# Optimization experiments

Hardware: AMD Instinct MI355X
Metric: run time of the kernel (lower is better)

The kernel has to match this reference:

```python
import jax, jax.numpy as jnp
import numpy as np

C = 64
OUT_Z = 32
HW = 128
NUM_HEADS = 4
COMP = 16          # max(c//reduction, num_heads) = 64//4
HEAD_DIM = COMP // NUM_HEADS
MAX_Z = 32
GROWTH = 16
NEG_SLOPE = 0.2


def setup_inputs() -> dict:
    key = jax.random.key(0)
    ks = jax.random.split(key, 16)
    ch = OUT_Z * C  # 2048

    def nrm(k, shape, std):
        return (jax.random.normal(k, shape, jnp.float32) * std).astype(jnp.float32)

    inp = {
        "trans_feature": jax.random.normal(ks[0], (1, ch, HW, HW), jnp.float32),
        "ln_w": jnp.ones((C,), jnp.float32),
        "ln_b": jnp.zeros((C,), jnp.float32),
        "wq": nrm(ks[1], (C, COMP), 0.05), "bq": jnp.zeros((COMP,), jnp.float32),
        "wk": nrm(ks[2], (C, COMP), 0.05), "bk": jnp.zeros((COMP,), jnp.float32),
        "wv": nrm(ks[3], (C, COMP), 0.05), "bv": jnp.zeros((COMP,), jnp.float32),
        "wo": nrm(ks[4], (COMP, C), 0.05), "bo": jnp.zeros((C,), jnp.float32),
        "rel_z_bias": nrm(ks[5], (NUM_HEADS, 2 * MAX_Z + 1), 0.02),
        "attn_gamma": jnp.asarray(0.1, jnp.float32),
        "dw0": nrm(ks[6], (ch + 0 * GROWTH, GROWTH), 0.02), "db0": jnp.zeros((GROWTH,), jnp.float32),
        "dw1": nrm(ks[7], (ch + 1 * GROWTH, GROWTH), 0.02), "db1": jnp.zeros((GROWTH,), jnp.float32),
        "dw2": nrm(ks[8], (ch + 2 * GROWTH, GROWTH), 0.02), "db2": jnp.zeros((GROWTH,), jnp.float32),
        "fuse_w": nrm(ks[9], (ch + 3 * GROWTH, ch), 0.02), "fuse_b": jnp.zeros((ch,), jnp.float32),
        "rdc_scale": jnp.asarray(0.1, jnp.float32),
        "out_z": OUT_Z,
    }
    return inp


def _conv1x1(x, w, b):
    # 1x1 conv == per-pixel dense: x [B,Cin,H,W], w [Cin,Cout]
    return jnp.einsum('bchw,co->bohw', x, w) + b[None, :, None, None]


def _lrelu(x):
    return jnp.where(x >= 0, x, NEG_SLOPE * x)


def reference(trans_feature, ln_w, ln_b, wq, bq, wk, bk, wv, bv, wo, bo,
              rel_z_bias, attn_gamma, dw0, db0, dw1, db1, dw2, db2,
              fuse_w, fuse_b, rdc_scale, out_z):
    B, Ct, H, W = trans_feature.shape
    c = Ct // out_z
    # ---- ZAxisAttention on slices [out_z, c, H, W] ----
    x = trans_feature.reshape(out_z, c, H, W)
    xf = x.transpose(0, 2, 3, 1).reshape(out_z, H * W, c)   # [Z, N, c]
    mu = xf.mean(-1, keepdims=True)
    var = ((xf - mu) ** 2).mean(-1, keepdims=True)
    normed = (xf - mu) * jax.lax.rsqrt(var + 1e-5) * ln_w + ln_b
    pooled = normed.mean(1)                                  # [Z, c]
    q = (pooled @ wq + bq).reshape(out_z, NUM_HEADS, HEAD_DIM).transpose(1, 0, 2)
    k = (pooled @ wk + bk).reshape(out_z, NUM_HEADS, HEAD_DIM).transpose(1, 0, 2)
    v = (pooled @ wv + bv).reshape(out_z, NUM_HEADS, HEAD_DIM).transpose(1, 0, 2)
    attn = jnp.einsum('hid,hjd->hij', q, k) * (HEAD_DIM ** -0.5)  # [h, Z, Z]
    zr = jnp.arange(out_z)
    rel_idx = jnp.clip(zr[None, :] - zr[:, None] + MAX_Z, 0, 2 * MAX_Z)
    attn = jax.nn.softmax(attn + rel_z_bias[:, rel_idx], axis=-1)
    o = jnp.einsum('hij,hjd->hid', attn, v).transpose(1, 0, 2).reshape(out_z, COMP)
    o = o @ wo + bo                                          # [Z, c]
    x_z = (x + attn_gamma * o[:, :, None, None]).reshape(B, Ct, H, W)
    # ---- ResidualDenseBlock on full [B, Ct, H, W] (out_z == max_out_z) ----
    feats = trans_feature
    f0 = _lrelu(_conv1x1(feats, dw0, db0))
    feats = jnp.concatenate([feats, f0], axis=1)
    f1 = _lrelu(_conv1x1(feats, dw1, db1))
    feats = jnp.concatenate([feats, f1], axis=1)
    f2 = _lrelu(_conv1x1(feats, dw2, db2))
    feats = jnp.concatenate([feats, f2], axis=1)
    fused = _lrelu(_conv1x1(feats, fuse_w, fuse_b))
    x_rdc = trans_feature + rdc_scale * fused
    return x_z + x_rdc - trans_feature
```

## Files before the change

### kernel.cpp

```cpp
#include <hip/hip_runtime.h>
#include <hip/hip_fp8.h>

typedef unsigned char u8;
typedef unsigned short u16;
typedef long lng2 __attribute__((ext_vector_type(2)));
typedef float f32x4 __attribute__((ext_vector_type(4)));
typedef u16 u16x8 __attribute__((ext_vector_type(8)));
typedef u8 u8x16 __attribute__((ext_vector_type(16)));

#define HW_N 16384
#define NCH  2048

__device__ __forceinline__ u16 f2bf(float f) {
  union { float f; unsigned u; } v; v.f = f;
  unsigned r = v.u + 0x7FFFu + ((v.u >> 16) & 1u);
  return (u16)(r >> 16);
}
__device__ __forceinline__ float bf2f(u16 u) {
  union { unsigned u; float f; } v; v.u = ((unsigned)u) << 16; return v.f;
}
__device__ __forceinline__ u8 f2fp8(float f) {
  __hip_fp8_e4m3 t(f);
  return (u8)t.__x;
}
__device__ __forceinline__ float lrelu(float v) { return v >= 0.0f ? v : 0.2f * v; }

__device__ __forceinline__ void gload_lds16(const u8* g, u8* l) {
  __builtin_amdgcn_global_load_lds((const __attribute__((address_space(1))) void*)g,
                                   (__attribute__((address_space(3))) void*)l, 16, 0, 0);
}

__global__ __launch_bounds__(256) void k_stats(const float* __restrict__ trans,
                                               u8* __restrict__ A8,
                                               float* __restrict__ pooled_sum) {
  const int z = blockIdx.x;
  const int tid = threadIdx.x;
  const int ptile = blockIdx.y;
  const int p = ptile * 256 + tid;
  const float* src = trans + (size_t)z * 64 * HW_N + p;
  float x[64];
#pragma unroll
  for (int c = 0; c < 64; ++c) x[c] = src[(size_t)c * HW_N];
  float sum = 0.f, sq = 0.f;
#pragma unroll
  for (int c = 0; c < 64; ++c) { sum += x[c]; sq += x[c] * x[c]; }
  const float mu = sum * (1.0f / 64.0f);
  const float var = sq * (1.0f / 64.0f) - mu * mu;
  const float rstd = rsqrtf(var + 1e-5f);

  __shared__ __align__(16) u8 rawt[256 * 64];
  __shared__ __align__(16) u16 normt[256 * 64];
  const int r3m = tid & 3, r7 = tid & 7;
#pragma unroll
  for (int c = 0; c < 4; ++c) {
    u8x16 y;
#pragma unroll
    for (int w = 0; w < 16; ++w) {
      const int k = (w < 8) ? (c * 8 + w) : (32 + c * 8 + (w - 8));
      y[w] = f2fp8(x[k]);
    }
    *(u8x16*)&rawt[tid * 64 + ((c ^ r3m) << 4)] = y;
  }
#pragma unroll
  for (int c8 = 0; c8 < 8; ++c8) {
    u16x8 wn;
#pragma unroll
    for (int e = 0; e < 8; ++e) wn[e] = f2bf((x[c8 * 8 + e] - mu) * rstd);
    *(u16x8*)&normt[tid * 64 + ((c8 ^ r7) << 3)] = wn;
  }
  __syncthreads();

  u8* gbase = A8 + ((size_t)z * HW_N + (size_t)ptile * 256) * 64;
#pragma unroll
  for (int it = 0; it < 4; ++it) {
    const int o = it * 256 + tid;
    const int row = o >> 2, c4 = o & 3;
    *(u8x16*)(gbase + o * 16) = *(const u8x16*)&rawt[row * 64 + ((c4 ^ (row & 3)) << 4)];
  }

  const int c = tid & 63, q = tid >> 6;
  const int kc2 = c >> 3, e2 = c & 7;
  float s = 0.f;
#pragma unroll 8
  for (int i = 0; i < 64; ++i) {
    const int row = q * 64 + i;
    s += bf2f(normt[row * 64 + ((kc2 ^ (row & 7)) << 3) + e2]);
  }
  __shared__ float red2[4][64];
  red2[q][c] = s;
  __syncthreads();
  if (tid < 64) {
    atomicAdd(&pooled_sum[z * 64 + tid],
              red2[0][tid] + red2[1][tid] + red2[2][tid] + red2[3][tid]);
  }
}

__global__ __launch_bounds__(256) void k_wpack(const float* __restrict__ fw,
                                               const float* __restrict__ dw0,
                                               const float* __restrict__ dw1,
                                               const float* __restrict__ dw2,
                                               u8* __restrict__ W8,
                                               u8* __restrict__ Wd8) {
  __shared__ float tile[64][65];
  const int tid = threadIdx.x;
  const int ktile = blockIdx.x;
  const int yb = blockIdx.y;
  if (yb == 32) {
    const int kc = ktile;
    if (kc >= 32) return;
    for (int idx = tid; idx < 3072; idx += 256) {
      const int kk = idx / 48, j = idx % 48;
      const int k = kc * 64 + kk;
      float v = (j < 16) ? dw0[k * 16 + j]
              : (j < 32) ? dw1[k * 16 + (j - 16)]
                         : dw2[k * 16 + (j - 32)];
      tile[kk][j] = v;
    }
    __syncthreads();
    for (int idx = tid; idx < 3072; idx += 256) {
      const int j = idx / 64, kk = idx % 64;
      const int pos = ((kk >> 3) & 3) * 16 + (kk & 7) + ((kk >> 5) << 3);
      Wd8[((size_t)kc * 48 + j) * 64 + pos] = f2fp8(16.0f * tile[kk][j]);
    }
    return;
  }
  const int ntile = yb;
  {
    const int kk0 = tid >> 6, nn = tid & 63;
#pragma unroll
    for (int it = 0; it < 16; ++it) {
      int kk = it * 4 + kk0;
      int kg = ktile * 64 + kk;
      tile[kk][nn] = (kg < 2096) ? fw[(size_t)kg * NCH + ntile * 64 + nn] : 0.0f;
    }
  }
  __syncthreads();
  {
    const int kk = tid & 63, nn0 = tid >> 6;
    const int pos = ((kk >> 3) & 3) * 16 + (kk & 7) + ((kk >> 5) << 3);
#pragma unroll
    for (int it = 0; it < 16; ++it) {
      int n = it * 4 + nn0;
      W8[((size_t)ktile * NCH + ntile * 64 + n) * 64 + pos] = f2fp8(16.0f * tile[kk][n]);
    }
  }
}

__global__ __launch_bounds__(256) void k_dense(const u8* __restrict__ A8,
    const u8* __restrict__ Wd8,
    const float* __restrict__ dw1, const float* __restrict__ dw2,
    const float* __restrict__ db0, const float* __restrict__ db1,
    const float* __restrict__ db2, u8* __restrict__ A8out) {
  __shared__ __align__(16) u8 lsA[128 * 64];
  __shared__ __align__(16) u8 lsW[48 * 64];
  __shared__ float trn[128][49];
  __shared__ float w1t[16][16];
  __shared__ float w2t[32][16];
  __shared__ float biases[48];
  const int tid = threadIdx.x;
  const int lane = tid & 63;
  const int wave = __builtin_amdgcn_readfirstlane(tid >> 6);
  const int mb = blockIdx.x;
  const int r16 = lane & 15, kgrp = lane >> 4;
  const int sgoff8 = ((lane >> 2) << 6) + (((lane & 3) ^ ((lane >> 3) & 3)) << 4);
  const int kx = (kgrp ^ ((r16 >> 1) & 3)) << 4;

  if (tid < 256) w1t[tid >> 4][tid & 15] = dw1[(2048 + (tid >> 4)) * 16 + (tid & 15)];
  for (int idx = tid; idx < 512; idx += 256)
    w2t[idx >> 4][idx & 15] = dw2[(2048 + (idx >> 4)) * 16 + (idx & 15)];
  if (tid < 48) biases[tid] = (tid < 16) ? db0[tid] : (tid < 32) ? db1[tid - 16] : db2[tid - 32];

  f32x4 acc[3][2] = {};
  for (int t = 0; t < 32; ++t) {
    const u8* slabA = A8 + ((size_t)t * HW_N + (size_t)mb * 128) * 64;
    const u8* slabW = Wd8 + (size_t)t * 48 * 64;
#pragma unroll
    for (int p = 0; p < 2; ++p)
      gload_lds16(slabA + (p * 4 + wave) * 1024 + sgoff8, lsA + (p * 4 + wave) * 1024);
    if (wave < 3)
      gload_lds16(slabW + wave * 1024 + sgoff8, lsW + wave * 1024);
    asm volatile("s_waitcnt vmcnt(0)" ::: "memory");
    __syncthreads();

    lng2 wf[3], af[2];
#pragma unroll
    for (int f = 0; f < 3; ++f)
      wf[f] = *(const lng2*)(lsW + (f * 16 + r16) * 64 + kx);
#pragma unroll
    for (int g = 0; g < 2; ++g)
      af[g] = *(const lng2*)(lsA + (wave * 32 + g * 16 + r16) * 64 + kx);
#pragma unroll
    for (int f = 0; f < 3; ++f)
#pragma unroll
      for (int g = 0; g < 2; ++g) {
        acc[f][g] = __builtin_amdgcn_mfma_f32_16x16x32_fp8_fp8(wf[f][0], af[g][0], acc[f][g], 0, 0, 0);
        acc[f][g] = __builtin_amdgcn_mfma_f32_16x16x32_fp8_fp8(wf[f][1], af[g][1], acc[f][g], 0, 0, 0);
      }
    __syncthreads();
  }

  const int rg = lane >> 4;
#pragma unroll
  for (int f = 0; f < 3; ++f)
#pragma unroll
    for (int r = 0; r < 4; ++r)
#pragma unroll
      for (int g = 0; g < 2; ++g)
        trn[wave * 32 + g * 16 + r16][f * 16 + rg * 4 + r] = acc[f][g][r] * 0.0625f;
  __syncthreads();

  if (tid < 128) {
    float gv[48];
#pragma unroll
    for (int j = 0; j < 48; ++j) gv[j] = trn[tid][j];
    float f0[16], f1[16], f2[16];
#pragma unroll
    for (int j = 0; j < 16; ++j) f0[j] = lrelu(gv[j] + biases[j]);
#pragma unroll
    for (int j = 0; j < 16; ++j) {
      float a = gv[16 + j] + biases[16 + j];
#pragma unroll
      for (int i = 0; i < 16; ++i) a += f0[i] * w1t[i][j];
      f1[j] = lrelu(a);
    }
#pragma unroll
    for (int j = 0; j < 16; ++j) {
      float a = gv[32 + j] + biases[32 + j];
#pragma unroll
      for (int i = 0; i < 16; ++i) a += f0[i] * w2t[i][j];
#pragma unroll
      for (int i = 0; i < 16; ++i) a += f1[i] * w2t[16 + i][j];
      f2[j] = lrelu(a);
    }
    u8* dst = A8out + ((size_t)32 * HW_N + mb * 128 + tid) * 64;
#pragma unroll
    for (int c = 0; c < 4; ++c) {
      u8x16 y;
#pragma unroll
      for (int w = 0; w < 16; ++w) {
        const int k = (w < 8) ? (c * 8 + w) : (32 + c * 8 + (w - 8));
        const float v = (k < 16) ? f0[k] : (k < 32) ? f1[k - 16] : (k < 48) ? f2[k - 32] : 0.0f;
        y[w] = f2fp8(v);
      }
      *(u8x16*)(dst + c * 16) = y;
    }
  }
}

__global__ __launch_bounds__(256) void k_attn(const float* __restrict__ pooled_sum,
    const float* __restrict__ ln_w, const float* __restrict__ ln_b,
    const float* __restrict__ wq, const float* __restrict__ bq,
    const float* __restrict__ wk, const float* __restrict__ bk,
    const float* __restrict__ wv, const float* __restrict__ bv,
    const float* __restrict__ wo, const float* __restrict__ bo,
    const float* __restrict__ relz, const float* __restrict__ attn_gamma,
    float* __restrict__ o_scaled) {
  __shared__ float pooled[2048];
  __shared__ float q[512], k[512], v[512], att[4096], tz[512];
  const int tid = threadIdx.x;
  for (int i = tid; i < 2048; i += 256) {
    int c = i & 63;
    pooled[i] = ln_w[c] * pooled_sum[i] * (1.0f / 16384.0f) + ln_b[c];
  }
  __syncthreads();
  for (int i = tid; i < 512; i += 256) {
    int z = i >> 4, e = i & 15;
    float aq = bq[e], ak = bk[e], av = bv[e];
    for (int c = 0; c < 64; ++c) {
      float p = pooled[z * 64 + c];
      aq += p * wq[c * 16 + e]; ak += p * wk[c * 16 + e]; av += p * wv[c * 16 + e];
    }
    q[i] = aq; k[i] = ak; v[i] = av;
  }
  __syncthreads();
  if (tid < 128) {
    int h = tid >> 5, zi = tid & 31;
    float s[32]; float mx = -1e30f;
#pragma unroll
    for (int j = 0; j < 32; ++j) {
      float d = 0.f;
#pragma unroll
      for (int e = 0; e < 4; ++e) d += q[zi * 16 + h * 4 + e] * k[j * 16 + h * 4 + e];
      d = d * 0.5f + relz[h * 65 + (j - zi + 32)];
      s[j] = d; mx = fmaxf(mx, d);
    }
    float ssum = 0.f;
#pragma unroll
    for (int j = 0; j < 32; ++j) { s[j] = __expf(s[j] - mx); ssum += s[j]; }
    float inv = 1.0f / ssum;
#pragma unroll
    for (int j = 0; j < 32; ++j) att[(h * 32 + zi) * 32 + j] = s[j] * inv;
  }
  __syncthreads();
  for (int i = tid; i < 512; i += 256) {
    int z = i >> 4, hd = i & 15, h = hd >> 2;
    float a = 0.f;
    for (int j = 0; j < 32; ++j) a += att[(h * 32 + z) * 32 + j] * v[j * 16 + hd];
    tz[i] = a;
  }
  __syncthreads();
  const float gamma = attn_gamma[0];
  for (int i = tid; i < 2048; i += 256) {
    int z = i >> 6, c = i & 63;
    float a = bo[c];
    for (int hd = 0; hd < 16; ++hd) a += tz[z * 16 + hd] * wo[hd * 64 + c];
    o_scaled[i] = gamma * a;
  }
}

__global__ __launch_bounds__(512, 2) void k_gemm(
    const u8* __restrict__ A8, const u8* __restrict__ W8,
    const float* __restrict__ trans, const float* __restrict__ o_scaled,
    const float* __restrict__ fuse_b, const float* __restrict__ rdc_scale,
    float* __restrict__ out) {
  __shared__ __align__(16) u8 ls[65536];
  const int tid = threadIdx.x;
  const int lane = tid & 63;
  const int wave = __builtin_amdgcn_readfirstlane(tid >> 6);
  const int bid = blockIdx.x;
  const int nb = bid & 7;
  const int mb = bid >> 3;
  const int mbase = mb * 256, nbase = nb * 256;
  const int wm = wave & 1;
  const int wn = wave >> 1;
  const int wnh = wn >> 1;
  const int wrow = (wn & 1) * 64;
  const int r16 = lane & 15, kgrp = lane >> 4;
  const int sgoff8 = ((lane >> 2) << 6) + (((lane & 3) ^ ((lane >> 3) & 3)) << 4);
  const int kx = (kgrp ^ ((r16 >> 1) & 3)) << 4;

#define LA(b, h) (ls + (b) * 32768 + (h) * 8192)
#define LW(b, h) (ls + (b) * 32768 + 16384 + (h) * 8192)
#define AHALF(t, h) (A8 + ((size_t)(t) * HW_N + mbase + (h) * 128) * 64)
#define WHALF(t, h) (W8 + ((size_t)(t) * NCH + nbase + (h) * 128) * 64)
#define STAGE(rows, ldsh) gload_lds16((rows) + wave * 1024 + sgoff8, (ldsh) + wave * 1024)
#define RD8(base, row) (*(const lng2*)((base) + (row) * 64 + kx))
#define MF8(a, b, c) __builtin_amdgcn_mfma_f32_16x16x32_fp8_fp8((a), (b), (c), 0, 0, 0)

  f32x4 acc[4][8] = {};
  lng2 wf0a[2], afLa[4];
  lng2 wf0b[2], afLb[4];

  STAGE(WHALF(0, 0), LW(0, 0));
  STAGE(WHALF(0, 1), LW(0, 1));
  STAGE(AHALF(0, 0), LA(0, 0));
  STAGE(AHALF(0, 1), LA(0, 1));
  asm volatile("s_waitcnt vmcnt(0)" ::: "memory");
  __builtin_amdgcn_s_barrier();
  {
    const u8* lw0 = LW(0, wnh);
    const u8* la0 = LA(0, wm);
#pragma unroll
    for (int f = 0; f < 2; ++f) wf0a[f] = RD8(lw0, wrow + f * 16 + r16);
#pragma unroll
    for (int g = 0; g < 4; ++g) afLa[g] = RD8(la0, g * 16 + r16);
  }

#define GBODY(T, W0C, ALC, W0N, ALN)                                           \
  {                                                                            \
    const int t = (T);                                                         \
    const int buf = t & 1, nbf = buf ^ 1;                                      \
    const int tn = (t + 1 < 33) ? t + 1 : 32;                                  \
    const u8* la = LA(buf, wm);                                                \
    const u8* lw = LW(buf, wnh);                                               \
    lng2 wf1[2], afH[4];                                                       \
                            \
    _Pragma("unroll") for (int f = 0; f < 2; ++f)                              \
      wf1[f] = RD8(lw, wrow + 32 + f * 16 + r16);                              \
    STAGE(WHALF(tn, 0), LW(nbf, 0));                                           \
    STAGE(WHALF(tn, 1), LW(nbf, 1));                                           \
    __builtin_amdgcn_s_setprio(1);                                             \
    _Pragma("unroll") for (int f = 0; f < 2; ++f)                              \
      _Pragma("unroll") for (int g = 0; g < 4; ++g) {                          \
        acc[f][g] = MF8(W0C[f][0], ALC[g][0], acc[f][g]);                      \
        acc[f][g] = MF8(W0C[f][1], ALC[g][1], acc[f][g]);                      \
      }                                                                        \
    __builtin_amdgcn_s_setprio(0);                                             \
                            \
    _Pragma("unroll") for (int g = 0; g < 4; ++g)                              \
      afH[g] = RD8(la, 64 + g * 16 + r16);                                     \
    STAGE(AHALF(tn, 0), LA(nbf, 0));                                           \
    STAGE(AHALF(tn, 1), LA(nbf, 1));                                           \
    __builtin_amdgcn_s_setprio(1);                                             \
    _Pragma("unroll") for (int f = 0; f < 2; ++f)                              \
      _Pragma("unroll") for (int g = 0; g < 4; ++g) {                          \
        acc[2 + f][g] = MF8(wf1[f][0], ALC[g][0], acc[2 + f][g]);              \
        acc[2 + f][g] = MF8(wf1[f][1], ALC[g][1], acc[2 + f][g]);              \
      }                                                                        \
    __builtin_amdgcn_s_setprio(0);                                             \
                                            \
    __builtin_amdgcn_s_setprio(1);                                             \
    _Pragma("unroll") for (int f = 0; f < 2; ++f)                              \
      _Pragma("unroll") for (int g = 0; g < 4; ++g) {                          \
        acc[2 + f][4 + g] = MF8(wf1[f][0], afH[g][0], acc[2 + f][4 + g]);      \
        acc[2 + f][4 + g] = MF8(wf1[f][1], afH[g][1], acc[2 + f][4 + g]);      \
      }                                                                        \
    __builtin_amdgcn_s_setprio(0);                                             \
            \
    asm volatile("s_waitcnt vmcnt(0)" ::: "memory");                           \
    __builtin_amdgcn_s_barrier();                                              \
    {                                                                          \
      const u8* lan = LA(nbf, wm);                                             \
      const u8* lwn = LW(nbf, wnh);                                            \
      _Pragma("unroll") for (int f = 0; f < 2; ++f)                            \
        W0N[f] = RD8(lwn, wrow + f * 16 + r16);                                \
      _Pragma("unroll") for (int g = 0; g < 4; ++g)                            \
        ALN[g] = RD8(lan, g * 16 + r16);                                       \
    }                                                                          \
    __builtin_amdgcn_s_setprio(1);                                             \
    _Pragma("unroll") for (int f = 0; f < 2; ++f)                              \
      _Pragma("unroll") for (int g = 0; g < 4; ++g) {                          \
        acc[f][4 + g] = MF8(W0C[f][0], afH[g][0], acc[f][4 + g]);              \
        acc[f][4 + g] = MF8(W0C[f][1], afH[g][1], acc[f][4 + g]);              \
      }                                                                        \
    __builtin_amdgcn_s_setprio(0);                                             \
  }

  for (int u = 0; u < 16; ++u) {
    GBODY(2 * u, wf0a, afLa, wf0b, afLb);
    GBODY(2 * u + 1, wf0b, afLb, wf0a, afLa);
  }
  GBODY(32, wf0a, afLa, wf0b, afLb);

  asm volatile("s_waitcnt vmcnt(0)" ::: "memory");

  const float rdc = rdc_scale[0];
  const int rg = lane >> 4;
#pragma unroll
  for (int f = 0; f < 4; ++f) {
#pragma unroll
    for (int r = 0; r < 4; ++r) {
      const int row = nbase + wn * 64 + f * 16 + rg * 4 + r;
      const float ob = o_scaled[row], fb = fuse_b[row];
#pragma unroll
      for (int g = 0; g < 8; ++g) {
        const int col = mbase + wm * 128 + g * 16 + r16;
        float v = lrelu(acc[f][g][r] * 0.0625f + fb);
        const size_t idx = (size_t)row * HW_N + col;
        out[idx] = trans[idx] + rdc * v + ob;
      }
    }
  }
#undef GBODY
#undef LA
#undef LW
#undef AHALF
#undef WHALF
#undef STAGE
#undef RD8
#undef MF8
}

extern "C" void kernel_launch(void* const* d_in, const int* in_sizes, int n_in,
                              void* d_out, int out_size, void* d_ws, size_t ws_size,
                              hipStream_t stream) {
  (void)in_sizes; (void)n_in; (void)out_size; (void)ws_size;
  const float* trans = (const float*)d_in[0];
  const float* ln_w  = (const float*)d_in[1];
  const float* ln_b  = (const float*)d_in[2];
  const float* wq = (const float*)d_in[3];  const float* bq = (const float*)d_in[4];
  const float* wk = (const float*)d_in[5];  const float* bk = (const float*)d_in[6];
  const float* wv = (const float*)d_in[7];  const float* bv = (const float*)d_in[8];
  const float* wo = (const float*)d_in[9];  const float* bo = (const float*)d_in[10];
  const float* relz  = (const float*)d_in[11];
  const float* gamma = (const float*)d_in[12];
  const float* dw0 = (const float*)d_in[13]; const float* db0 = (const float*)d_in[14];
  const float* dw1 = (const float*)d_in[15]; const float* db1 = (const float*)d_in[16];
  const float* dw2 = (const float*)d_in[17]; const float* db2 = (const float*)d_in[18];
  const float* fuse_w = (const float*)d_in[19];
  const float* fuse_b = (const float*)d_in[20];
  const float* rdc    = (const float*)d_in[21];
  float* out = (float*)d_out;

  char* ws = (char*)d_ws;
  u8*    A8         = (u8*)ws;
  u8*    W8         = (u8*)(ws + 34603008);
  u8*    Wd8        = (u8*)(ws + 38928384);
  float* pooled_sum = (float*)(ws + 39026688);
  float* o_scaled   = (float*)(ws + 39034880);

  hipMemsetAsync(pooled_sum, 0, 2048 * sizeof(float), stream);
  k_stats<<<dim3(32, 64), 256, 0, stream>>>(trans, A8, pooled_sum);
  k_wpack<<<dim3(33, 33), 256, 0, stream>>>(fuse_w, dw0, dw1, dw2, W8, Wd8);
  k_dense<<<dim3(128), 256, 0, stream>>>(A8, Wd8, dw1, dw2, db0, db1, db2, A8);
  k_attn<<<dim3(1), 256, 0, stream>>>(pooled_sum, ln_w, ln_b, wq, bq, wk, bk, wv, bv,
                                      wo, bo, relz, gamma, o_scaled);
  k_gemm<<<dim3(512), 512, 0, stream>>>(A8, W8, trans, o_scaled, fuse_b, rdc, out);
}
```

Measured before the change: 206.1 us.

## Switch FP8 GEMMs to 16x16x128 scaled MFMA with 128-byte K slabs

Repacks the activations and weights into 128-wide K slabs with an XOR-swizzled LDS layout. The dense and fused GEMMs now use the gfx950 mfma_scale 16x16x128 f8f6f4 instruction, which cuts the MFMA issue count and the number of K iterations. The hand-pipelined, double-buffered k_gemm loop is replaced by a simple single-buffered load/wait/compute loop, so global loads no longer overlap with MFMA work. Two extra memsets zero the padding slabs.

```diff
diff --git a/kernel.cpp b/kernel.cpp
--- a/kernel.cpp
+++ b/kernel.cpp
@@ -3,7 +3,8 @@
 
 typedef unsigned char u8;
 typedef unsigned short u16;
-typedef long lng2 __attribute__((ext_vector_type(2)));
+typedef int i32x4 __attribute__((ext_vector_type(4)));
+typedef int i32x8 __attribute__((ext_vector_type(8)));
 typedef float f32x4 __attribute__((ext_vector_type(4)));
 typedef u16 u16x8 __attribute__((ext_vector_type(8)));
 typedef u8 u8x16 __attribute__((ext_vector_type(16)));
@@ -30,8 +31,19 @@
                                    (__attribute__((address_space(3))) void*)l, 16, 0, 0);
 }
 
+#define MFS(a, b, c) \
+  __builtin_amdgcn_mfma_scale_f32_16x16x128_f8f6f4((a), (b), (c), 0, 0, 0, 0x7F7F7F7F, 0, 0x7F7F7F7F)
+
+#define RDFRAG(R, row, kg_, outv)                                              \
+  {                                                                            \
+    const int off_ = ((row) << 7) + ((((kg_) << 1) ^ ((row) & 7)) << 4);       \
+    i32x4 lo_ = *(const i32x4*)((R) + off_);                                   \
+    i32x4 hi_ = *(const i32x4*)((R) + (off_ ^ 16));                            \
+    outv = __builtin_shufflevector(lo_, hi_, 0, 1, 2, 3, 4, 5, 6, 7);          \
+  }
+
 __global__ __launch_bounds__(256) void k_stats(const float* __restrict__ trans,
-                                               u8* __restrict__ A8,
+                                               u8* __restrict__ A16,
                                                float* __restrict__ pooled_sum) {
   const int z = blockIdx.x;
   const int tid = threadIdx.x;
@@ -55,10 +67,7 @@
   for (int c = 0; c < 4; ++c) {
     u8x16 y;
 #pragma unroll
-    for (int w = 0; w < 16; ++w) {
-      const int k = (w < 8) ? (c * 8 + w) : (32 + c * 8 + (w - 8));
-      y[w] = f2fp8(x[k]);
-    }
+    for (int w = 0; w < 16; ++w) y[w] = f2fp8(x[c * 16 + w]);
     *(u8x16*)&rawt[tid * 64 + ((c ^ r3m) << 4)] = y;
   }
 #pragma unroll
@@ -70,12 +79,13 @@
   }
   __syncthreads();
 
-  u8* gbase = A8 + ((size_t)z * HW_N + (size_t)ptile * 256) * 64;
+  u8* gbase = A16 + ((size_t)(z >> 1) * HW_N + (size_t)ptile * 256) * 128 + (z & 1) * 64;
 #pragma unroll
   for (int it = 0; it < 4; ++it) {
     const int o = it * 256 + tid;
     const int row = o >> 2, c4 = o & 3;
-    *(u8x16*)(gbase + o * 16) = *(const u8x16*)&rawt[row * 64 + ((c4 ^ (row & 3)) << 4)];
+    *(u8x16*)(gbase + (size_t)row * 128 + c4 * 16) =
+        *(const u8x16*)&rawt[row * 64 + ((c4 ^ (row & 3)) << 4)];
   }
 
   const int c = tid & 63, q = tid >> 6;
@@ -99,8 +109,8 @@
                                                const float* __restrict__ dw0,
                                                const float* __restrict__ dw1,
                                                const float* __restrict__ dw2,
-                                               u8* __restrict__ W8,
-                                               u8* __restrict__ Wd8) {
+                                               u8* __restrict__ W16,
+                                               u8* __restrict__ Wd16) {
   __shared__ float tile[64][65];
   const int tid = threadIdx.x;
   const int ktile = blockIdx.x;
@@ -119,8 +129,7 @@
     __syncthreads();
     for (int idx = tid; idx < 3072; idx += 256) {
       const int j = idx / 64, kk = idx % 64;
-      const int pos = ((kk >> 3) & 3) * 16 + (kk & 7) + ((kk >> 5) << 3);
-      Wd8[((size_t)kc * 48 + j) * 64 + pos] = f2fp8(16.0f * tile[kk][j]);
+      Wd16[((size_t)(kc >> 1) * 48 + j) * 128 + (kc & 1) * 64 + kk] = f2fp8(16.0f * tile[kk][j]);
     }
     return;
   }
@@ -137,22 +146,22 @@
   __syncthreads();
   {
     const int kk = tid & 63, nn0 = tid >> 6;
-    const int pos = ((kk >> 3) & 3) * 16 + (kk & 7) + ((kk >> 5) << 3);
 #pragma unroll
     for (int it = 0; it < 16; ++it) {
       int n = it * 4 + nn0;
-      W8[((size_t)ktile * NCH + ntile * 64 + n) * 64 + pos] = f2fp8(16.0f * tile[kk][n]);
-    }
-  }
-}
-
-__global__ __launch_bounds__(256) void k_dense(const u8* __restrict__ A8,
-    const u8* __restrict__ Wd8,
+      W16[((size_t)(ktile >> 1) * NCH + ntile * 64 + n) * 128 + (ktile & 1) * 64 + kk] =
+          f2fp8(16.0f * tile[kk][n]);
+    }
+  }
+}
+
+__global__ __launch_bounds__(256) void k_dense(const u8* __restrict__ A16,
+    const u8* __restrict__ Wd16,
     const float* __restrict__ dw1, const float* __restrict__ dw2,
     const float* __restrict__ db0, const float* __restrict__ db1,
-    const float* __restrict__ db2, u8* __restrict__ A8out) {
-  __shared__ __align__(16) u8 lsA[128 * 64];
-  __shared__ __align__(16) u8 lsW[48 * 64];
+    const float* __restrict__ db2, u8* __restrict__ A16out) {
+  __shared__ __align__(16) u8 lsA[128 * 128];
+  __shared__ __align__(16) u8 lsW[48 * 128];
   __shared__ float trn[128][49];
   __shared__ float w1t[16][16];
   __shared__ float w2t[32][16];
@@ -161,9 +170,9 @@
   const int lane = tid & 63;
   const int wave = __builtin_amdgcn_readfirstlane(tid >> 6);
   const int mb = blockIdx.x;
-  const int r16 = lane & 15, kgrp = lane >> 4;
-  const int sgoff8 = ((lane >> 2) << 6) + (((lane & 3) ^ ((lane >> 3) & 3)) << 4);
-  const int kx = (kgrp ^ ((r16 >> 1) & 3)) << 4;
+  const int r16 = lane & 15, kg = lane >> 4;
+  const int srow8 = lane >> 3;
+  const int schunk = (((lane & 7) ^ srow8) << 4);
 
   if (tid < 256) w1t[tid >> 4][tid & 15] = dw1[(2048 + (tid >> 4)) * 16 + (tid & 15)];
   for (int idx = tid; idx < 512; idx += 256)
@@ -171,31 +180,34 @@
   if (tid < 48) biases[tid] = (tid < 16) ? db0[tid] : (tid < 32) ? db1[tid - 16] : db2[tid - 32];
 
   f32x4 acc[3][2] = {};
-  for (int t = 0; t < 32; ++t) {
-    const u8* slabA = A8 + ((size_t)t * HW_N + (size_t)mb * 128) * 64;
-    const u8* slabW = Wd8 + (size_t)t * 48 * 64;
-#pragma unroll
-    for (int p = 0; p < 2; ++p)
-      gload_lds16(slabA + (p * 4 + wave) * 1024 + sgoff8, lsA + (p * 4 + wave) * 1024);
-    if (wave < 3)
-      gload_lds16(slabW + wave * 1024 + sgoff8, lsW + wave * 1024);
+  for (int t = 0; t < 16; ++t) {
+    const u8* Asl = A16 + ((size_t)t * HW_N + (size_t)mb * 128) * 128;
+    const u8* Wsl = Wd16 + (size_t)t * 48 * 128;
+#pragma unroll
+    for (int i = 0; i < 4; ++i) {
+      const int r0 = wave * 32 + i * 8;
+      gload_lds16(Asl + (size_t)(r0 + srow8) * 128 + schunk, lsA + r0 * 128 + lane * 16);
+    }
+    if (wave < 3) {
+#pragma unroll
+      for (int i = 0; i < 2; ++i) {
+        const int r0 = wave * 16 + i * 8;
+        gload_lds16(Wsl + (size_t)(r0 + srow8) * 128 + schunk, lsW + r0 * 128 + lane * 16);
+      }
+    }
     asm volatile("s_waitcnt vmcnt(0)" ::: "memory");
     __syncthreads();
 
-    lng2 wf[3], af[2];
+    i32x8 wf[3], af[2];
+#pragma unroll
+    for (int f = 0; f < 3; ++f) RDFRAG(lsW, f * 16 + r16, kg, wf[f]);
+#pragma unroll
+    for (int g = 0; g < 2; ++g) RDFRAG(lsA, wave * 32 + g * 16 + r16, kg, af[g]);
 #pragma unroll
     for (int f = 0; f < 3; ++f)
-      wf[f] = *(const lng2*)(lsW + (f * 16 + r16) * 64 + kx);
-#pragma unroll
-    for (int g = 0; g < 2; ++g)
-      af[g] = *(const lng2*)(lsA + (wave * 32 + g * 16 + r16) * 64 + kx);
-#pragma unroll
-    for (int f = 0; f < 3; ++f)
-#pragma unroll
-      for (int g = 0; g < 2; ++g) {
-        acc[f][g] = __builtin_amdgcn_mfma_f32_16x16x32_fp8_fp8(wf[f][0], af[g][0], acc[f][g], 0, 0, 0);
-        acc[f][g] = __builtin_amdgcn_mfma_f32_16x16x32_fp8_fp8(wf[f][1], af[g][1], acc[f][g], 0, 0, 0);
-      }
+#pragma unroll
+      for (int g = 0; g < 2; ++g)
+        acc[f][g] = MFS(wf[f], af[g], acc[f][g]);
     __syncthreads();
   }
 
@@ -232,14 +244,14 @@
       for (int i = 0; i < 16; ++i) a += f1[i] * w2t[16 + i][j];
       f2[j] = lrelu(a);
     }
-    u8* dst = A8out + ((size_t)32 * HW_N + mb * 128 + tid) * 64;
-#pragma unroll
-    for (int c = 0; c < 4; ++c) {
+    u8* dst = A16out + ((size_t)16 * HW_N + mb * 128 + tid) * 128;
+#pragma unroll
+    for (int c = 0; c < 3; ++c) {
       u8x16 y;
 #pragma unroll
       for (int w = 0; w < 16; ++w) {
-        const int k = (w < 8) ? (c * 8 + w) : (32 + c * 8 + (w - 8));
-        const float v = (k < 16) ? f0[k] : (k < 32) ? f1[k - 16] : (k < 48) ? f2[k - 32] : 0.0f;
+        const int k = c * 16 + w;
+        const float v = (k < 16) ? f0[k] : (k < 32) ? f1[k - 16] : f2[k - 32];
         y[w] = f2fp8(v);
       }
       *(u8x16*)(dst + c * 16) = y;
@@ -309,7 +321,7 @@
 }
 
 __global__ __launch_bounds__(512, 2) void k_gemm(
-    const u8* __restrict__ A8, const u8* __restrict__ W8,
+    const u8* __restrict__ A16, const u8* __restrict__ W16,
     const float* __restrict__ trans, const float* __restrict__ o_scaled,
     const float* __restrict__ fuse_b, const float* __restrict__ rdc_scale,
     float* __restrict__ out) {
@@ -323,106 +335,45 @@
   const int mbase = mb * 256, nbase = nb * 256;
   const int wm = wave & 1;
   const int wn = wave >> 1;
-  const int wnh = wn >> 1;
-  const int wrow = (wn & 1) * 64;
-  const int r16 = lane & 15, kgrp = lane >> 4;
-  const int sgoff8 = ((lane >> 2) << 6) + (((lane & 3) ^ ((lane >> 3) & 3)) << 4);
-  const int kx = (kgrp ^ ((r16 >> 1) & 3)) << 4;
-
-#define LA(b, h) (ls + (b) * 32768 + (h) * 8192)
-#define LW(b, h) (ls + (b) * 32768 + 16384 + (h) * 8192)
-#define AHALF(t, h) (A8 + ((size_t)(t) * HW_N + mbase + (h) * 128) * 64)
-#define WHALF(t, h) (W8 + ((size_t)(t) * NCH + nbase + (h) * 128) * 64)
-#define STAGE(rows, ldsh) gload_lds16((rows) + wave * 1024 + sgoff8, (ldsh) + wave * 1024)
-#define RD8(base, row) (*(const lng2*)((base) + (row) * 64 + kx))
-#define MF8(a, b, c) __builtin_amdgcn_mfma_f32_16x16x32_fp8_fp8((a), (b), (c), 0, 0, 0)
+  const int r16 = lane & 15, kg = lane >> 4;
+  const int srow8 = lane >> 3;
+  const int schunk = (((lane & 7) ^ srow8) << 4);
+  u8* const lsA = ls;
+  u8* const lsW = ls + 32768;
 
   f32x4 acc[4][8] = {};
-  lng2 wf0a[2], afLa[4];
-  lng2 wf0b[2], afLb[4];
-
-  STAGE(WHALF(0, 0), LW(0, 0));
-  STAGE(WHALF(0, 1), LW(0, 1));
-  STAGE(AHALF(0, 0), LA(0, 0));
-  STAGE(AHALF(0, 1), LA(0, 1));
-  asm volatile("s_waitcnt vmcnt(0)" ::: "memory");
-  __builtin_amdgcn_s_barrier();
-  {
-    const u8* lw0 = LW(0, wnh);
-    const u8* la0 = LA(0, wm);
-#pragma unroll
-    for (int f = 0; f < 2; ++f) wf0a[f] = RD8(lw0, wrow + f * 16 + r16);
-#pragma unroll
-    for (int g = 0; g < 4; ++g) afLa[g] = RD8(la0, g * 16 + r16);
-  }
-
-#define GBODY(T, W0C, ALC, W0N, ALN)                                           \
-  {                                                                            \
-    const int t = (T);                                                         \
-    const int buf = t & 1, nbf = buf ^ 1;                                      \
-    const int tn = (t + 1 < 33) ? t + 1 : 32;                                  \
-    const u8* la = LA(buf, wm);                                                \
-    const u8* lw = LW(buf, wnh);                                               \
-    lng2 wf1[2], afH[4];                                                       \
-                            \
-    _Pragma("unroll") for (int f = 0; f < 2; ++f)                              \
-      wf1[f] = RD8(lw, wrow + 32 + f * 16 + r16);                              \
-    STAGE(WHALF(tn, 0), LW(nbf, 0));                                           \
-    STAGE(WHALF(tn, 1), LW(nbf, 1));                                           \
-    __builtin_amdgcn_s_setprio(1);                                             \
-    _Pragma("unroll") for (int f = 0; f < 2; ++f)                              \
-      _Pragma("unroll") for (int g = 0; g < 4; ++g) {                          \
-        acc[f][g] = MF8(W0C[f][0], ALC[g][0], acc[f][g]);                      \
-        acc[f][g] = MF8(W0C[f][1], ALC[g][1], acc[f][g]);                      \
-      }                                                                        \
-    __builtin_amdgcn_s_setprio(0);                                             \
-                            \
-    _Pragma("unroll") for (int g = 0; g < 4; ++g)                              \
-      afH[g] = RD8(la, 64 + g * 16 + r16);                                     \
-    STAGE(AHALF(tn, 0), LA(nbf, 0));                                           \
-    STAGE(AHALF(tn, 1), LA(nbf, 1));                                           \
-    __builtin_amdgcn_s_setprio(1);                                             \
-    _Pragma("unroll") for (int f = 0; f < 2; ++f)                              \
-      _Pragma("unroll") for (int g = 0; g < 4; ++g) {                          \
-        acc[2 + f][g] = MF8(wf1[f][0], ALC[g][0], acc[2 + f][g]);              \
-        acc[2 + f][g] = MF8(wf1[f][1], ALC[g][1], acc[2 + f][g]);              \
-      }                                                                        \
-    __builtin_amdgcn_s_setprio(0);                                             \
-                                            \
-    __builtin_amdgcn_s_setprio(1);                                             \
-    _Pragma("unroll") for (int f = 0; f < 2; ++f)                              \
-      _Pragma("unroll") for (int g = 0; g < 4; ++g) {                          \
-        acc[2 + f][4 + g] = MF8(wf1[f][0], afH[g][0], acc[2 + f][4 + g]);      \
-        acc[2 + f][4 + g] = MF8(wf1[f][1], afH[g][1], acc[2 + f][4 + g]);      \
-      }                                                                        \
-    __builtin_amdgcn_s_setprio(0);                                             \
-            \
-    asm volatile("s_waitcnt vmcnt(0)" ::: "memory");                           \
-    __builtin_amdgcn_s_barrier();                                              \
-    {                                                                          \
-      const u8* lan = LA(nbf, wm);                                             \
-      const u8* lwn = LW(nbf, wnh);                                            \
-      _Pragma("unroll") for (int f = 0; f < 2; ++f)                            \
-        W0N[f] = RD8(lwn, wrow + f * 16 + r16);                                \
-      _Pragma("unroll") for (int g = 0; g < 4; ++g)                            \
-        ALN[g] = RD8(lan, g * 16 + r16);                                       \
-    }                                                                          \
-    __builtin_amdgcn_s_setprio(1);                                             \
-    _Pragma("unroll") for (int f = 0; f < 2; ++f)                              \
-      _Pragma("unroll") for (int g = 0; g < 4; ++g) {                          \
-        acc[f][4 + g] = MF8(W0C[f][0], afH[g][0], acc[f][4 + g]);              \
-        acc[f][4 + g] = MF8(W0C[f][1], afH[g][1], acc[f][4 + g]);              \
-      }                                                                        \
-    __builtin_amdgcn_s_setprio(0);                                             \
-  }
-
-  for (int u = 0; u < 16; ++u) {
-    GBODY(2 * u, wf0a, afLa, wf0b, afLb);
-    GBODY(2 * u + 1, wf0b, afLb, wf0a, afLa);
-  }
-  GBODY(32, wf0a, afLa, wf0b, afLb);
-
-  asm volatile("s_waitcnt vmcnt(0)" ::: "memory");
+
+  for (int t = 0; t < 17; ++t) {
+    const u8* Asl = A16 + ((size_t)t * HW_N + mbase) * 128;
+    const u8* Wsl = W16 + ((size_t)t * NCH + nbase) * 128;
+#pragma unroll
+    for (int i = 0; i < 4; ++i) {
+      const int r0 = wave * 32 + i * 8;
+      gload_lds16(Asl + (size_t)(r0 + srow8) * 128 + schunk, lsA + r0 * 128 + lane * 16);
+    }
+#pragma unroll
+    for (int i = 0; i < 4; ++i) {
+      const int r0 = wave * 32 + i * 8;
+      gload_lds16(Wsl + (size_t)(r0 + srow8) * 128 + schunk, lsW + r0 * 128 + lane * 16);
+    }
+    asm volatile("s_waitcnt vmcnt(0)" ::: "memory");
+    __builtin_amdgcn_s_barrier();
+
+    i32x8 wf[4];
+#pragma unroll
+    for (int f = 0; f < 4; ++f) RDFRAG(lsW, wn * 64 + f * 16 + r16, kg, wf[f]);
+    __builtin_amdgcn_s_setprio(1);
+#pragma unroll
+    for (int g = 0; g < 8; ++g) {
+      i32x8 af;
+      RDFRAG(lsA, wm * 128 + g * 16 + r16, kg, af);
+#pragma unroll
+      for (int f = 0; f < 4; ++f)
+        acc[f][g] = MFS(wf[f], af, acc[f][g]);
+    }
+    __builtin_amdgcn_s_setprio(0);
+    __builtin_amdgcn_s_barrier();
+  }
 
   const float rdc = rdc_scale[0];
   const int rg = lane >> 4;
@@ -441,14 +392,6 @@
       }
     }
   }
-#undef GBODY
-#undef LA
-#undef LW
-#undef AHALF
-#undef WHALF
-#undef STAGE
-#undef RD8
-#undef MF8
 }
 
 extern "C" void kernel_launch(void* const* d_in, const int* in_sizes, int n_in,
@@ -473,17 +416,19 @@
   float* out = (float*)d_out;
 
   char* ws = (char*)d_ws;
-  u8*    A8         = (u8*)ws;
-  u8*    W8         = (u8*)(ws + 34603008);
-  u8*    Wd8        = (u8*)(ws + 38928384);
-  float* pooled_sum = (float*)(ws + 39026688);
-  float* o_scaled   = (float*)(ws + 39034880);
+  u8*    A16        = (u8*)ws;
+  u8*    W16        = (u8*)(ws + 35651584);
+  u8*    Wd16       = (u8*)(ws + 40108032);
+  float* pooled_sum = (float*)(ws + 40206336);
+  float* o_scaled   = (float*)(ws + 40214528);
 
   hipMemsetAsync(pooled_sum, 0, 2048 * sizeof(float), stream);
-  k_stats<<<dim3(32, 64), 256, 0, stream>>>(trans, A8, pooled_sum);
-  k_wpack<<<dim3(33, 33), 256, 0, stream>>>(fuse_w, dw0, dw1, dw2, W8, Wd8);
-  k_dense<<<dim3(128), 256, 0, stream>>>(A8, Wd8, dw1, dw2, db0, db1, db2, A8);
+  hipMemsetAsync(A16 + (size_t)16 * HW_N * 128, 0, (size_t)HW_N * 128, stream);
+  hipMemsetAsync(W16 + (size_t)16 * NCH * 128, 0, (size_t)NCH * 128, stream);
+  k_stats<<<dim3(32, 64), 256, 0, stream>>>(trans, A16, pooled_sum);
+  k_wpack<<<dim3(33, 33), 256, 0, stream>>>(fuse_w, dw0, dw1, dw2, W16, Wd16);
+  k_dense<<<dim3(128), 256, 0, stream>>>(A16, Wd16, dw1, dw2, db0, db1, db2, A16);
   k_attn<<<dim3(1), 256, 0, stream>>>(pooled_sum, ln_w, ln_b, wq, bq, wk, bk, wv, bv,
                                       wo, bo, relz, gamma, o_scaled);
-  k_gemm<<<dim3(512), 512, 0, stream>>>(A8, W8, trans, o_scaled, fuse_b, rdc, out);
-}
+  k_gemm<<<dim3(512), 512, 0, stream>>>(A16, W16, trans, o_scaled, fuse_b, rdc, out);
+}
```

Measured after the change: 212.0 us. +2.9%, slower.

## Retile fp8 fuse GEMM to 128x256 blocks with 4 waves and 3 blocks/CU

Applied to the files above, without the earlier changes.

The main fp8 MFMA GEMM changes from 256x256 tiles with 8 waves per block to 128(pixel)x256(channel) tiles with 4 waves per block, launching 1024 blocks. Each wave now computes 64x128 outputs and keeps 4 channel and 4 pixel fragments resident. LDS per block shrinks to 48KB so three blocks can share a CU. The aim is better occupancy and load balance across the 256 CUs. The cost is less operand reuse per block, so more global and LDS traffic per MFMA.

```diff
diff --git a/kernel.cpp b/kernel.cpp
--- a/kernel.cpp
+++ b/kernel.cpp
@@ -308,133 +308,127 @@
   }
 }
 
-__global__ __launch_bounds__(512, 2) void k_gemm(
+__global__ __launch_bounds__(256, 3) void k_gemm(
     const u8* __restrict__ A8, const u8* __restrict__ W8,
     const float* __restrict__ trans, const float* __restrict__ o_scaled,
     const float* __restrict__ fuse_b, const float* __restrict__ rdc_scale,
     float* __restrict__ out) {
-  __shared__ __align__(16) u8 ls[65536];
+  __shared__ __align__(16) u8 ls[49152];
   const int tid = threadIdx.x;
   const int lane = tid & 63;
   const int wave = __builtin_amdgcn_readfirstlane(tid >> 6);
   const int bid = blockIdx.x;
   const int nb = bid & 7;
   const int mb = bid >> 3;
-  const int mbase = mb * 256, nbase = nb * 256;
+  const int mbase = mb * 128, nbase = nb * 256;
   const int wm = wave & 1;
   const int wn = wave >> 1;
-  const int wnh = wn >> 1;
-  const int wrow = (wn & 1) * 64;
+  const int prow = wm * 64;
+  const int crow = wn * 128;
   const int r16 = lane & 15, kgrp = lane >> 4;
   const int sgoff8 = ((lane >> 2) << 6) + (((lane & 3) ^ ((lane >> 3) & 3)) << 4);
   const int kx = (kgrp ^ ((r16 >> 1) & 3)) << 4;
 
-#define LA(b, h) (ls + (b) * 32768 + (h) * 8192)
-#define LW(b, h) (ls + (b) * 32768 + 16384 + (h) * 8192)
-#define AHALF(t, h) (A8 + ((size_t)(t) * HW_N + mbase + (h) * 128) * 64)
-#define WHALF(t, h) (W8 + ((size_t)(t) * NCH + nbase + (h) * 128) * 64)
-#define STAGE(rows, ldsh) gload_lds16((rows) + wave * 1024 + sgoff8, (ldsh) + wave * 1024)
+#define LA(b) (ls + (b) * 24576)
+#define LW(b) (ls + (b) * 24576 + 8192)
+#define ATILE(t) (A8 + ((size_t)(t) * HW_N + mbase) * 64)
+#define WTILE(t) (W8 + ((size_t)(t) * NCH + nbase) * 64)
+#define STA(t, b)                                                              \
+  do {                                                                         \
+    gload_lds16(ATILE(t) + wave * 1024 + sgoff8, LA(b) + wave * 1024);         \
+    gload_lds16(ATILE(t) + 4096 + wave * 1024 + sgoff8, LA(b) + 4096 + wave * 1024); \
+  } while (0)
+#define STW(t, b)                                                              \
+  do {                                                                         \
+    _Pragma("unroll") for (int i_ = 0; i_ < 4; ++i_)                           \
+      gload_lds16(WTILE(t) + (i_ * 4 + wave) * 1024 + sgoff8,                  \
+                  LW(b) + (i_ * 4 + wave) * 1024);                             \
+  } while (0)
 #define RD8(base, row) (*(const lng2*)((base) + (row) * 64 + kx))
 #define MF8(a, b, c) __builtin_amdgcn_mfma_f32_16x16x32_fp8_fp8((a), (b), (c), 0, 0, 0)
 
-  f32x4 acc[4][8] = {};
-  lng2 wf0a[2], afLa[4];
-  lng2 wf0b[2], afLb[4];
-
-  STAGE(WHALF(0, 0), LW(0, 0));
-  STAGE(WHALF(0, 1), LW(0, 1));
-  STAGE(AHALF(0, 0), LA(0, 0));
-  STAGE(AHALF(0, 1), LA(0, 1));
+  f32x4 acc[8][4] = {};
+  lng2 cfa[4], pfa[4];
+  lng2 cfb[4], pfb[4];
+
+  STA(0, 0);
+  STW(0, 0);
   asm volatile("s_waitcnt vmcnt(0)" ::: "memory");
   __builtin_amdgcn_s_barrier();
-  {
-    const u8* lw0 = LW(0, wnh);
-    const u8* la0 = LA(0, wm);
-#pragma unroll
-    for (int f = 0; f < 2; ++f) wf0a[f] = RD8(lw0, wrow + f * 16 + r16);
-#pragma unroll
-    for (int g = 0; g < 4; ++g) afLa[g] = RD8(la0, g * 16 + r16);
-  }
-
-#define GBODY(T, W0C, ALC, W0N, ALN)                                           \
+#pragma unroll
+  for (int f = 0; f < 4; ++f) cfa[f] = RD8(LW(0), crow + f * 16 + r16);
+#pragma unroll
+  for (int g = 0; g < 4; ++g) pfa[g] = RD8(LA(0), prow + g * 16 + r16);
+
+#define GBODY(T, CFC, PFC, CFN, PFN)                                           \
   {                                                                            \
     const int t = (T);                                                         \
     const int buf = t & 1, nbf = buf ^ 1;                                      \
     const int tn = (t + 1 < 33) ? t + 1 : 32;                                  \
-    const u8* la = LA(buf, wm);                                                \
-    const u8* lw = LW(buf, wnh);                                               \
-    lng2 wf1[2], afH[4];                                                       \
+    lng2 cf47[4];                                                              \
                             \
-    _Pragma("unroll") for (int f = 0; f < 2; ++f)                              \
-      wf1[f] = RD8(lw, wrow + 32 + f * 16 + r16);                              \
-    STAGE(WHALF(tn, 0), LW(nbf, 0));                                           \
-    STAGE(WHALF(tn, 1), LW(nbf, 1));                                           \
+    _Pragma("unroll") for (int f = 0; f < 4; ++f)                              \
+      cf47[f] = RD8(LW(buf), crow + 64 + f * 16 + r16);                        \
+    STA(tn, nbf);                                                              \
     __builtin_amdgcn_s_setprio(1);                                             \
     _Pragma("unroll") for (int f = 0; f < 2; ++f)                              \
       _Pragma("unroll") for (int g = 0; g < 4; ++g) {                          \
-        acc[f][g] = MF8(W0C[f][0], ALC[g][0], acc[f][g]);                      \
-        acc[f][g] = MF8(W0C[f][1], ALC[g][1], acc[f][g]);                      \
+        acc[f][g] = MF8(CFC[f][0], PFC[g][0], acc[f][g]);                      \
+        acc[f][g] = MF8(CFC[f][1], PFC[g][1], acc[f][g]);                      \
       }                                                                        \
     __builtin_amdgcn_s_setprio(0);                                             \
-                            \
-    _Pragma("unroll") for (int g = 0; g < 4; ++g)                              \
-      afH[g] = RD8(la, 64 + g * 16 + r16);                                     \
-    STAGE(AHALF(tn, 0), LA(nbf, 0));                                           \
-    STAGE(AHALF(tn, 1), LA(nbf, 1));                                           \
+                                          \
+    STW(tn, nbf);                                                              \
     __builtin_amdgcn_s_setprio(1);                                             \
     _Pragma("unroll") for (int f = 0; f < 2; ++f)                              \
       _Pragma("unroll") for (int g = 0; g < 4; ++g) {                          \
-        acc[2 + f][g] = MF8(wf1[f][0], ALC[g][0], acc[2 + f][g]);              \
-        acc[2 + f][g] = MF8(wf1[f][1], ALC[g][1], acc[2 + f][g]);              \
+        acc[2 + f][g] = MF8(CFC[2 + f][0], PFC[g][0], acc[2 + f][g]);          \
+        acc[2 + f][g] = MF8(CFC[2 + f][1], PFC[g][1], acc[2 + f][g]);          \
       }                                                                        \
     __builtin_amdgcn_s_setprio(0);                                             \
-                                            \
+                                             \
     __builtin_amdgcn_s_setprio(1);                                             \
     _Pragma("unroll") for (int f = 0; f < 2; ++f)                              \
       _Pragma("unroll") for (int g = 0; g < 4; ++g) {                          \
-        acc[2 + f][4 + g] = MF8(wf1[f][0], afH[g][0], acc[2 + f][4 + g]);      \
-        acc[2 + f][4 + g] = MF8(wf1[f][1], afH[g][1], acc[2 + f][4 + g]);      \
+        acc[4 + f][g] = MF8(cf47[f][0], PFC[g][0], acc[4 + f][g]);             \
+        acc[4 + f][g] = MF8(cf47[f][1], PFC[g][1], acc[4 + f][g]);             \
       }                                                                        \
     __builtin_amdgcn_s_setprio(0);                                             \
             \
     asm volatile("s_waitcnt vmcnt(0)" ::: "memory");                           \
     __builtin_amdgcn_s_barrier();                                              \
-    {                                                                          \
-      const u8* lan = LA(nbf, wm);                                             \
-      const u8* lwn = LW(nbf, wnh);                                            \
-      _Pragma("unroll") for (int f = 0; f < 2; ++f)                            \
-        W0N[f] = RD8(lwn, wrow + f * 16 + r16);                                \
-      _Pragma("unroll") for (int g = 0; g < 4; ++g)                            \
-        ALN[g] = RD8(lan, g * 16 + r16);                                       \
-    }                                                                          \
+    _Pragma("unroll") for (int f = 0; f < 4; ++f)                              \
+      CFN[f] = RD8(LW(nbf), crow + f * 16 + r16);                              \
+    _Pragma("unroll") for (int g = 0; g < 4; ++g)                              \
+      PFN[g] = RD8(LA(nbf), prow + g * 16 + r16);                              \
     __builtin_amdgcn_s_setprio(1);                                             \
     _Pragma("unroll") for (int f = 0; f < 2; ++f)                              \
       _Pragma("unroll") for (int g = 0; g < 4; ++g) {                          \
-        acc[f][4 + g] = MF8(W0C[f][0], afH[g][0], acc[f][4 + g]);              \
-        acc[f][4 + g] = MF8(W0C[f][1], afH[g][1], acc[f][4 + g]);              \
+        acc[6 + f][g] = MF8(cf47[2 + f][0], PFC[g][0], acc[6 + f][g]);         \
+        acc[6 + f][g] = MF8(cf47[2 + f][1], PFC[g][1], acc[6 + f][g]);         \
       }                                                                        \
     __builtin_amdgcn_s_setprio(0);                                             \
   }
 
   for (int u = 0; u < 16; ++u) {
-    GBODY(2 * u, wf0a, afLa, wf0b, afLb);
-    GBODY(2 * u + 1, wf0b, afLb, wf0a, afLa);
-  }
-  GBODY(32, wf0a, afLa, wf0b, afLb);
+    GBODY(2 * u, cfa, pfa, cfb, pfb);
+    GBODY(2 * u + 1, cfb, pfb, cfa, pfa);
+  }
+  GBODY(32, cfa, pfa, cfb, pfb);
 
   asm volatile("s_waitcnt vmcnt(0)" ::: "memory");
 
   const float rdc = rdc_scale[0];
   const int rg = lane >> 4;
 #pragma unroll
-  for (int f = 0; f < 4; ++f) {
+  for (int f = 0; f < 8; ++f) {
 #pragma unroll
     for (int r = 0; r < 4; ++r) {
-      const int row = nbase + wn * 64 + f * 16 + rg * 4 + r;
+      const int row = nbase + crow + f * 16 + rg * 4 + r;
       const float ob = o_scaled[row], fb = fuse_b[row];
 #pragma unroll
-      for (int g = 0; g < 8; ++g) {
-        const int col = mbase + wm * 128 + g * 16 + r16;
+      for (int g = 0; g < 4; ++g) {
+        const int col = mbase + prow + g * 16 + r16;
         float v = lrelu(acc[f][g][r] * 0.0625f + fb);
         const size_t idx = (size_t)row * HW_N + col;
         out[idx] = trans[idx] + rdc * v + ob;
@@ -444,9 +438,10 @@
 #undef GBODY
 #undef LA
 #undef LW
-#undef AHALF
-#undef WHALF
-#undef STAGE
+#undef ATILE
+#undef WTILE
+#undef STA
+#undef STW
 #undef RD8
 #undef MF8
 }
@@ -485,5 +480,5 @@
   k_dense<<<dim3(128), 256, 0, stream>>>(A8, Wd8, dw1, dw2, db0, db1, db2, A8);
   k_attn<<<dim3(1), 256, 0, stream>>>(pooled_sum, ln_w, ln_b, wq, bq, wk, bk, wv, bv,
                                       wo, bo, relz, gamma, o_scaled);
-  k_gemm<<<dim3(512), 512, 0, stream>>>(A8, W8, trans, o_scaled, fuse_b, rdc, out);
-}
+  k_gemm<<<dim3(1024), 256, 0, stream>>>(A8, W8, trans, o_scaled, fuse_b, rdc, out);
+}
```

New measurement: 610.5 us. +196.2%, slower.
